# Optimization experiments

Hardware: AMD Instinct MI355X
Metric: run time of the kernel (lower is better)

The kernel has to match this reference:

```python
import jax, jax.numpy as jnp
import numpy as np
from jax import lax

B_, L_, D_, N_, K_ = 2, 4096, 1024, 16, 4


def setup_inputs() -> dict:
    key = jax.random.key(0)
    ks = jax.random.split(key, 11)
    s = lambda fan: 1.0 / np.sqrt(fan)
    return {
        "x": jax.random.normal(ks[0], (B_, L_, D_), jnp.float32),
        "W_in": jax.random.normal(ks[1], (D_, 2 * D_), jnp.float32) * s(D_),
        "b_in": jax.random.normal(ks[2], (2 * D_,), jnp.float32) * 0.01,
        "conv_w": jax.random.normal(ks[3], (D_, K_), jnp.float32) * s(K_),
        "conv_b": jax.random.normal(ks[4], (D_,), jnp.float32) * 0.01,
        "W_x": jax.random.normal(ks[5], (D_, 2 * N_), jnp.float32) * s(D_),
        "b_x": jax.random.normal(ks[6], (2 * N_,), jnp.float32) * 0.01,
        "A_log": jax.random.normal(ks[7], (D_, N_), jnp.float32),
        "D_param": jnp.ones((D_,), jnp.float32),
        "W_out": jax.random.normal(ks[8], (D_, D_), jnp.float32) * s(D_),
        "b_out": jax.random.normal(ks[9], (D_,), jnp.float32) * 0.01,
    }


def silu(x):
    return x * jax.nn.sigmoid(x)


def s6_forward(x, W_in, b_in, conv_w, conv_b, W_x, b_x, A_log, D_param, W_out, b_out):
    b, L, D = x.shape
    # in_proj then split into ssm stream and gate
    x_and_gate = x @ W_in + b_in                      # [b, L, 2D]
    x_ssm, gate = jnp.split(x_and_gate, 2, axis=-1)   # each [b, L, D]

    # depthwise causal conv: padding=(d_conv-1, d_conv-1) then [:, :, :L] == left-pad only
    xc = jnp.transpose(x_ssm, (0, 2, 1))              # [b, D, L]
    xc = lax.conv_general_dilated(
        xc, conv_w[:, None, :],                       # [D, 1, K]
        window_strides=(1,), padding=[(K_ - 1, 0)],
        feature_group_count=D,
        dimension_numbers=("NCH", "OIH", "NCH"),
    ) + conv_b[None, :, None]
    x_conv = silu(jnp.transpose(xc, (0, 2, 1)))       # [b, L, D]

    # data-dependent B, C
    BC = x_conv @ W_x + b_x                           # [b, L, 2N]
    B_mat, C_mat = jnp.split(BC, 2, axis=-1)          # each [b, L, N]

    A_discrete = jnp.exp(-jnp.exp(A_log))             # [D, N]

    # sequential selective scan over L, carry h: [b, D, N]
    def step(h, inp):
        xc_t, B_t, C_t = inp                          # [b,D], [b,N], [b,N]
        h = A_discrete[None] * h + xc_t[:, :, None] * B_t[:, None, :]
        y = jnp.einsum("bn,bdn->bd", C_t, h) + D_param * xc_t
        return h, y

    h0 = jnp.zeros((b, D, N_), x.dtype)
    xs = (jnp.transpose(x_conv, (1, 0, 2)),
          jnp.transpose(B_mat, (1, 0, 2)),
          jnp.transpose(C_mat, (1, 0, 2)))
    h_final, ys = lax.scan(step, h0, xs)              # ys: [L, b, D]
    y = jnp.transpose(ys, (1, 0, 2))                  # [b, L, D]

    y = y * silu(gate)
    y = y @ W_out + b_out
    final_state = h_final.mean(axis=1)                # [b, N]
    return y, final_state


def reference(x, W_in, b_in, conv_w, conv_b, W_x, b_x, A_log, D_param, W_out, b_out):
    return s6_forward(x, W_in, b_in, conv_w, conv_b, W_x, b_x, A_log, D_param, W_out, b_out)
```

## Files before the change

### kernel.cpp

```cpp
#include <hip/hip_runtime.h>
#include <hip/hip_bf16.h>
#include <math.h>

#define LL 4096
#define DD 1024
#define NN 16
#define KK 4
#define BB 2
#define MM (BB * LL)
#define NC 64
#define LC 64

typedef unsigned short ushort_t;
typedef short s16x8 __attribute__((ext_vector_type(8)));
typedef float f32x4 __attribute__((ext_vector_type(4)));
typedef unsigned int u32;

__device__ __forceinline__ ushort_t f2bf(float f) {
  __hip_bfloat16 h = __float2bfloat16(f);
  return *reinterpret_cast<ushort_t*>(&h);
}

__global__ __launch_bounds__(256) void gemm_bt_mfma(
    const ushort_t* __restrict__ A,
    const ushort_t* __restrict__ BT,
    const float* __restrict__ bias,
    float* __restrict__ C, int N) {
  constexpr int K = 1024;
  __shared__ ushort_t As[128 * 32];
  __shared__ ushort_t Bs[128 * 32];

  const int tid = threadIdx.x;
  const int lane = tid & 63;
  const int w = tid >> 6;
  const int wm = w & 1, wn = w >> 1;
  const int row0 = blockIdx.y * 128;
  const int col0 = blockIdx.x * 128;

  const int lrow = lane >> 2;
  const int lk = (lane & 3) * 8;

  f32x4 acc[4][4];
#pragma unroll
  for (int i = 0; i < 4; ++i)
#pragma unroll
    for (int j = 0; j < 4; ++j) acc[i][j] = (f32x4){0.f, 0.f, 0.f, 0.f};

  const int frow = lane & 15;
  const int quad = lane >> 4;

  for (int k0 = 0; k0 < K; k0 += 32) {
#pragma unroll
    for (int it = 0; it < 2; ++it) {
      int r = it * 64 + w * 16;
      __builtin_amdgcn_global_load_lds(
          (const __attribute__((address_space(1))) u32*)(A + (size_t)(row0 + r + lrow) * K + k0 + lk),
          (__attribute__((address_space(3))) u32*)(As + r * 32), 16, 0, 0);
      __builtin_amdgcn_global_load_lds(
          (const __attribute__((address_space(1))) u32*)(BT + (size_t)(col0 + r + lrow) * K + k0 + lk),
          (__attribute__((address_space(3))) u32*)(Bs + r * 32), 16, 0, 0);
    }
    __syncthreads();

    s16x8 af[4], bf[4];
#pragma unroll
    for (int mi = 0; mi < 4; ++mi)
      af[mi] = *(const s16x8*)&As[(wm * 64 + mi * 16 + frow) * 32 + quad * 8];
#pragma unroll
    for (int ni = 0; ni < 4; ++ni)
      bf[ni] = *(const s16x8*)&Bs[(wn * 64 + ni * 16 + frow) * 32 + quad * 8];
#pragma unroll
    for (int mi = 0; mi < 4; ++mi)
#pragma unroll
      for (int ni = 0; ni < 4; ++ni)
        acc[mi][ni] = __builtin_amdgcn_mfma_f32_16x16x32_bf16(
            af[mi], bf[ni], acc[mi][ni], 0, 0, 0);
    __syncthreads();
  }

#pragma unroll
  for (int mi = 0; mi < 4; ++mi) {
#pragma unroll
    for (int ni = 0; ni < 4; ++ni) {
      int col = col0 + wn * 64 + ni * 16 + frow;
      float b = bias[col];
#pragma unroll
      for (int r = 0; r < 4; ++r) {
        int row = row0 + wm * 64 + mi * 16 + quad * 4 + r;
        C[(size_t)row * N + col] = acc[mi][ni][r] + b;
      }
    }
  }
}

__global__ __launch_bounds__(128) void bc_mfma_k(
    const ushort_t* __restrict__ A,
    const ushort_t* __restrict__ BT,
    const float* __restrict__ bias,
    float* __restrict__ C) {
  constexpr int K = 1024;
  __shared__ ushort_t As[32 * 32];
  __shared__ ushort_t Bs[32 * 32];

  const int tid = threadIdx.x;
  const int lane = tid & 63;
  const int w = tid >> 6;
  const int row0 = blockIdx.x * 32;
  const int lrow = lane >> 2;
  const int lk = (lane & 3) * 8;
  const int frow = lane & 15;
  const int quad = lane >> 4;

  f32x4 acc[2];
  acc[0] = (f32x4){0.f, 0.f, 0.f, 0.f};
  acc[1] = (f32x4){0.f, 0.f, 0.f, 0.f};

  for (int k0 = 0; k0 < K; k0 += 32) {
    __builtin_amdgcn_global_load_lds(
        (const __attribute__((address_space(1))) u32*)(A + (size_t)(row0 + w * 16 + lrow) * K + k0 + lk),
        (__attribute__((address_space(3))) u32*)(As + (w * 16) * 32), 16, 0, 0);
    __builtin_amdgcn_global_load_lds(
        (const __attribute__((address_space(1))) u32*)(BT + (size_t)(w * 16 + lrow) * K + k0 + lk),
        (__attribute__((address_space(3))) u32*)(Bs + (w * 16) * 32), 16, 0, 0);
    __syncthreads();

    s16x8 af = *(const s16x8*)&As[(w * 16 + frow) * 32 + quad * 8];
    s16x8 bf0 = *(const s16x8*)&Bs[(frow)*32 + quad * 8];
    s16x8 bf1 = *(const s16x8*)&Bs[(16 + frow) * 32 + quad * 8];
    acc[0] = __builtin_amdgcn_mfma_f32_16x16x32_bf16(af, bf0, acc[0], 0, 0, 0);
    acc[1] = __builtin_amdgcn_mfma_f32_16x16x32_bf16(af, bf1, acc[1], 0, 0, 0);
    __syncthreads();
  }

#pragma unroll
  for (int ni = 0; ni < 2; ++ni) {
    int col = ni * 16 + frow;
    float b = bias[col];
#pragma unroll
    for (int r = 0; r < 4; ++r) {
      int row = row0 + w * 16 + quad * 4 + r;
      C[(size_t)row * 32 + col] = acc[ni][r] + b;
    }
  }
}

__global__ __launch_bounds__(256) void cast_bf16_k(
    const float* __restrict__ src, ushort_t* __restrict__ dst) {
  int i = blockIdx.x * 256 + threadIdx.x;
  float4 v = ((const float4*)src)[i];
  ushort4 o;
  o.x = f2bf(v.x); o.y = f2bf(v.y); o.z = f2bf(v.z); o.w = f2bf(v.w);
  ((ushort4*)dst)[i] = o;
}

__global__ __launch_bounds__(256) void transpose_cast_k(
    const float* __restrict__ W, ushort_t* __restrict__ WT, int K, int N) {
  __shared__ float t[32][33];
  int nb = blockIdx.x * 32, kb = blockIdx.y * 32;
  int tx = threadIdx.x, ty = threadIdx.y;
#pragma unroll
  for (int i = 0; i < 32; i += 8)
    t[ty + i][tx] = W[(size_t)(kb + ty + i) * N + nb + tx];
  __syncthreads();
#pragma unroll
  for (int i = 0; i < 32; i += 8)
    WT[(size_t)(nb + ty + i) * K + kb + tx] = f2bf(t[tx][ty + i]);
}

__global__ __launch_bounds__(256) void conv_silu_k(
    const float* __restrict__ XG, const float* __restrict__ conv_w,
    const float* __restrict__ conv_b, float* __restrict__ XC,
    ushort_t* __restrict__ XCb) {
  int idx = blockIdx.x * 256 + threadIdx.x;
  int d = idx & (DD - 1);
  int m = idx >> 10;
  int b = m >> 12;
  int l = m & (LL - 1);
  float v = conv_b[d];
#pragma unroll
  for (int k = 0; k < KK; ++k) {
    int li = l + k - (KK - 1);
    if (li >= 0) v += XG[((size_t)(b * LL + li)) * 2048 + d] * conv_w[d * KK + k];
  }
  float s = v / (1.f + __expf(-v));
  XC[(size_t)m * DD + d] = s;
  XCb[(size_t)m * DD + d] = f2bf(s);
}

__global__ void zero_fs_k(float* fs) {
  if (threadIdx.x < 32) fs[threadIdx.x] = 0.f;
}

__global__ __launch_bounds__(64) void scan_local_k(
    const float* __restrict__ XC, const float* __restrict__ BC,
    const float* __restrict__ A_log, float* __restrict__ S) {
  const int b = blockIdx.x, c = blockIdx.y;
  const int tid = threadIdx.x;
  const int d = blockIdx.z * 64 + tid;
  const int t0 = c * LC;
  const size_t rowb = (size_t)b * LL;

  __shared__ float bc[LC * 32];
  {
    const float4* src = (const float4*)(BC + (rowb + t0) * 32);
    float4* dst = (float4*)bc;
#pragma unroll
    for (int i = 0; i < 8; ++i) dst[tid + i * 64] = src[tid + i * 64];
  }

  float a[NN], h[NN];
#pragma unroll
  for (int n = 0; n < NN; ++n) {
    a[n] = expf(-expf(A_log[d * NN + n]));
    h[n] = 0.f;
  }
  __syncthreads();

  const float* xp = XC + (rowb + t0) * DD + d;
  float xc = *xp;
  for (int t = 0; t < LC; ++t) {
    float xc_n = (t + 1 < LC) ? xp[(t + 1) * DD] : 0.f;
#pragma unroll
    for (int n = 0; n < NN; ++n) h[n] = a[n] * h[n] + xc * bc[t * 32 + n];
    xc = xc_n;
  }
  float* sp = S + (((size_t)(b * NC + c)) * DD + d) * NN;
#pragma unroll
  for (int n = 0; n < NN; ++n) sp[n] = h[n];
}

__global__ __launch_bounds__(256) void scan_carry_k(
    float* __restrict__ S, const float* __restrict__ A_log,
    float* __restrict__ fs) {
  const int idx = blockIdx.x * 256 + threadIdx.x;
  const int n = idx & (NN - 1);
  const int d = (idx / NN) & (DD - 1);
  const int b = idx / (NN * DD);

  const float aLC = expf(-(float)LC * expf(A_log[d * NN + n]));
  float h = 0.f;
  for (int c = 0; c < NC; ++c) {
    size_t off = (((size_t)(b * NC + c)) * DD + d) * NN + n;
    float s = S[off];
    S[off] = h;
    h = aLC * h + s;
  }
  __shared__ float red[256];
  red[threadIdx.x] = h * (1.f / (float)DD);
  __syncthreads();
  if (threadIdx.x < NN) {
    float sum = 0.f;
#pragma unroll
    for (int i = 0; i < 16; ++i) sum += red[i * NN + threadIdx.x];
    atomicAdd(&fs[b * NN + threadIdx.x], sum);
  }
}

__global__ __launch_bounds__(64) void scan_final_k(
    const float* __restrict__ XC, const float* __restrict__ XG,
    const float* __restrict__ BC, const float* __restrict__ A_log,
    const float* __restrict__ D_param, const float* __restrict__ H0,
    ushort_t* __restrict__ Y1b) {
  const int b = blockIdx.x, c = blockIdx.y;
  const int tid = threadIdx.x;
  const int d = blockIdx.z * 64 + tid;
  const int t0 = c * LC;
  const size_t rowb = (size_t)b * LL;

  __shared__ float bc[LC * 32];
  {
    const float4* src = (const float4*)(BC + (rowb + t0) * 32);
    float4* dst = (float4*)bc;
#pragma unroll
    for (int i = 0; i < 8; ++i) dst[tid + i * 64] = src[tid + i * 64];
  }

  float a[NN], h[NN];
  const float* hp = H0 + (((size_t)(b * NC + c)) * DD + d) * NN;
#pragma unroll
  for (int n = 0; n < NN; ++n) {
    a[n] = expf(-expf(A_log[d * NN + n]));
    h[n] = hp[n];
  }
  const float Dp = D_param[d];
  __syncthreads();

  const float* xp = XC + (rowb + t0) * DD + d;
  const float* gp = XG + (rowb + t0) * 2048 + DD + d;
  ushort_t* yp = Y1b + (rowb + t0) * DD + d;
  float xc = *xp, gate = *gp;
  for (int t = 0; t < LC; ++t) {
    float xc_n = 0.f, g_n = 0.f;
    if (t + 1 < LC) {
      xc_n = xp[(t + 1) * DD];
      g_n = gp[(t + 1) * 2048];
    }
    float y = Dp * xc;
#pragma unroll
    for (int n = 0; n < NN; ++n) {
      h[n] = a[n] * h[n] + xc * bc[t * 32 + n];
      y += bc[t * 32 + 16 + n] * h[n];
    }
    float sg = gate / (1.f + __expf(-gate));
    yp[t * DD] = f2bf(y * sg);
    xc = xc_n;
    gate = g_n;
  }
}

extern "C" void kernel_launch(void* const* d_in, const int* in_sizes, int n_in,
                              void* d_out, int out_size, void* d_ws,
                              size_t ws_size, hipStream_t stream) {
  const float* x = (const float*)d_in[0];
  const float* W_in = (const float*)d_in[1];
  const float* b_in = (const float*)d_in[2];
  const float* conv_w = (const float*)d_in[3];
  const float* conv_b = (const float*)d_in[4];
  const float* W_x = (const float*)d_in[5];
  const float* b_x = (const float*)d_in[6];
  const float* A_log = (const float*)d_in[7];
  const float* D_param = (const float*)d_in[8];
  const float* W_out = (const float*)d_in[9];
  const float* b_out = (const float*)d_in[10];
  float* out = (float*)d_out;

  float* XG = (float*)d_ws;
  float* XC = XG + (size_t)MM * 2048;
  float* BC = XC + (size_t)MM * DD;
  float* S = BC + (size_t)MM * 32;
  ushort_t* Xb = (ushort_t*)(S + (size_t)BB * NC * DD * NN);
  ushort_t* WinT = Xb + (size_t)MM * DD;
  ushort_t* WoutT = WinT + (size_t)2048 * DD;
  ushort_t* Y1b = WoutT + (size_t)DD * DD;
  ushort_t* XCb = Y1b + (size_t)MM * DD;
  ushort_t* WxT = XCb + (size_t)MM * DD;

  dim3 blk(256);
  cast_bf16_k<<<dim3((MM * DD) / 1024), blk, 0, stream>>>(x, Xb);
  transpose_cast_k<<<dim3(2048 / 32, 1024 / 32), dim3(32, 8), 0, stream>>>(
      W_in, WinT, 1024, 2048);
  transpose_cast_k<<<dim3(1024 / 32, 1024 / 32), dim3(32, 8), 0, stream>>>(
      W_out, WoutT, 1024, 1024);
  transpose_cast_k<<<dim3(1, 1024 / 32), dim3(32, 8), 0, stream>>>(
      W_x, WxT, 1024, 32);
  gemm_bt_mfma<<<dim3(2048 / 128, MM / 128), blk, 0, stream>>>(
      Xb, WinT, b_in, XG, 2048);
  conv_silu_k<<<dim3((MM * DD) / 256), blk, 0, stream>>>(XG, conv_w, conv_b,
                                                         XC, XCb);
  bc_mfma_k<<<dim3(MM / 32), dim3(128), 0, stream>>>(XCb, WxT, b_x, BC);
  scan_local_k<<<dim3(BB, NC, DD / 64), dim3(64), 0, stream>>>(XC, BC, A_log, S);
  zero_fs_k<<<dim3(1), dim3(64), 0, stream>>>(out + (size_t)MM * DD);
  scan_carry_k<<<dim3((BB * DD * NN) / 256), blk, 0, stream>>>(
      S, A_log, out + (size_t)MM * DD);
  scan_final_k<<<dim3(BB, NC, DD / 64), dim3(64), 0, stream>>>(
      XC, XG, BC, A_log, D_param, S, Y1b);
  gemm_bt_mfma<<<dim3(1024 / 128, MM / 128), blk, 0, stream>>>(
      Y1b, WoutT, b_out, out, 1024);
}
```

Baseline: 305.7 us.

## Store intermediates in bf16, vectorize conv, process two channels per scan thread

The in-projection GEMM now writes its output in bf16 instead of fp32. The conv kernel reads and writes only bf16 and handles 8 channels per thread with vector loads. The scan kernels read bf16 inputs and process two channels per thread, which halves the block count per chunk, and the fp32 XC/XG buffers are dropped. The zero-fill and three transpose launches are merged into fewer kernels. This cuts memory traffic on the largest intermediates and removes launches, at the cost of extra bf16 rounding on the gate and scan inputs and less parallelism in the scan.

```diff
diff --git a/kernel.cpp b/kernel.cpp
--- a/kernel.cpp
+++ b/kernel.cpp
@@ -20,12 +20,18 @@
   __hip_bfloat16 h = __float2bfloat16(f);
   return *reinterpret_cast<ushort_t*>(&h);
 }
-
+__device__ __forceinline__ float bf2f(ushort_t u) {
+  union { u32 i; float f; } c;
+  c.i = ((u32)u) << 16;
+  return c.f;
+}
+
+template <bool BF16OUT>
 __global__ __launch_bounds__(256) void gemm_bt_mfma(
     const ushort_t* __restrict__ A,
     const ushort_t* __restrict__ BT,
     const float* __restrict__ bias,
-    float* __restrict__ C, int N) {
+    void* __restrict__ Cv, int N) {
   constexpr int K = 1024;
   __shared__ ushort_t As[128 * 32];
   __shared__ ushort_t Bs[128 * 32];
@@ -87,7 +93,10 @@
 #pragma unroll
       for (int r = 0; r < 4; ++r) {
         int row = row0 + wm * 64 + mi * 16 + quad * 4 + r;
-        C[(size_t)row * N + col] = acc[mi][ni][r] + b;
+        if constexpr (BF16OUT)
+          ((ushort_t*)Cv)[(size_t)row * N + col] = f2bf(acc[mi][ni][r] + b);
+        else
+          ((float*)Cv)[(size_t)row * N + col] = acc[mi][ni][r] + b;
       }
     }
   }
@@ -145,7 +154,9 @@
 }
 
 __global__ __launch_bounds__(256) void cast_bf16_k(
-    const float* __restrict__ src, ushort_t* __restrict__ dst) {
+    const float* __restrict__ src, ushort_t* __restrict__ dst,
+    float* __restrict__ fs) {
+  if (blockIdx.x == 0 && threadIdx.x < 32) fs[threadIdx.x] = 0.f;
   int i = blockIdx.x * 256 + threadIdx.x;
   float4 v = ((const float4*)src)[i];
   ushort4 o;
@@ -153,8 +164,23 @@
   ((ushort4*)dst)[i] = o;
 }
 
-__global__ __launch_bounds__(256) void transpose_cast_k(
-    const float* __restrict__ W, ushort_t* __restrict__ WT, int K, int N) {
+__global__ void transpose_cast3_k(
+    const float* __restrict__ W_in, const float* __restrict__ W_out,
+    const float* __restrict__ W_x, ushort_t* __restrict__ WinT,
+    ushort_t* __restrict__ WoutT, ushort_t* __restrict__ WxT) {
+  constexpr int K = 1024;
+  const float* W;
+  ushort_t* WT;
+  int N;
+  if (blockIdx.z == 0) {
+    W = W_in; WT = WinT; N = 2048;
+  } else if (blockIdx.z == 1) {
+    if (blockIdx.x >= 32) return;
+    W = W_out; WT = WoutT; N = 1024;
+  } else {
+    if (blockIdx.x >= 1) return;
+    W = W_x; WT = WxT; N = 32;
+  }
   __shared__ float t[32][33];
   int nb = blockIdx.x * 32, kb = blockIdx.y * 32;
   int tx = threadIdx.x, ty = threadIdx.y;
@@ -168,65 +194,81 @@
 }
 
 __global__ __launch_bounds__(256) void conv_silu_k(
-    const float* __restrict__ XG, const float* __restrict__ conv_w,
-    const float* __restrict__ conv_b, float* __restrict__ XC,
-    ushort_t* __restrict__ XCb) {
-  int idx = blockIdx.x * 256 + threadIdx.x;
-  int d = idx & (DD - 1);
-  int m = idx >> 10;
-  int b = m >> 12;
+    const ushort_t* __restrict__ XGb, const float* __restrict__ conv_w,
+    const float* __restrict__ conv_b, ushort_t* __restrict__ XCb) {
+  int gid = blockIdx.x * 256 + threadIdx.x;
+  int m = gid >> 7;
+  int d0 = (gid & 127) * 8;
   int l = m & (LL - 1);
-  float v = conv_b[d];
+
+  float acc[8];
+#pragma unroll
+  for (int j = 0; j < 8; ++j) acc[j] = conv_b[d0 + j];
 #pragma unroll
   for (int k = 0; k < KK; ++k) {
     int li = l + k - (KK - 1);
-    if (li >= 0) v += XG[((size_t)(b * LL + li)) * 2048 + d] * conv_w[d * KK + k];
-  }
-  float s = v / (1.f + __expf(-v));
-  XC[(size_t)m * DD + d] = s;
-  XCb[(size_t)m * DD + d] = f2bf(s);
-}
-
-__global__ void zero_fs_k(float* fs) {
-  if (threadIdx.x < 32) fs[threadIdx.x] = 0.f;
+    if (li < 0) continue;
+    s16x8 v = *(const s16x8*)(XGb + (size_t)(m + k - (KK - 1)) * 2048 + d0);
+#pragma unroll
+    for (int j = 0; j < 8; ++j)
+      acc[j] += bf2f((ushort_t)v[j]) * conv_w[(d0 + j) * KK + k];
+  }
+  ushort_t o[8];
+#pragma unroll
+  for (int j = 0; j < 8; ++j) {
+    float s = acc[j] / (1.f + __expf(-acc[j]));
+    o[j] = f2bf(s);
+  }
+  *(s16x8*)(XCb + (size_t)m * DD + d0) = *(const s16x8*)o;
 }
 
 __global__ __launch_bounds__(64) void scan_local_k(
-    const float* __restrict__ XC, const float* __restrict__ BC,
+    const ushort_t* __restrict__ XCb, const float* __restrict__ BC,
     const float* __restrict__ A_log, float* __restrict__ S) {
   const int b = blockIdx.x, c = blockIdx.y;
   const int tid = threadIdx.x;
-  const int d = blockIdx.z * 64 + tid;
+  const int d0 = blockIdx.z * 128 + tid * 2;
   const int t0 = c * LC;
   const size_t rowb = (size_t)b * LL;
 
-  __shared__ float bc[LC * 32];
+  __shared__ float bcs[LC * 32];
   {
     const float4* src = (const float4*)(BC + (rowb + t0) * 32);
-    float4* dst = (float4*)bc;
+    float4* dst = (float4*)bcs;
 #pragma unroll
     for (int i = 0; i < 8; ++i) dst[tid + i * 64] = src[tid + i * 64];
   }
 
-  float a[NN], h[NN];
+  float a0[NN], a1[NN], h0[NN], h1[NN];
 #pragma unroll
   for (int n = 0; n < NN; ++n) {
-    a[n] = expf(-expf(A_log[d * NN + n]));
-    h[n] = 0.f;
+    a0[n] = expf(-expf(A_log[d0 * NN + n]));
+    a1[n] = expf(-expf(A_log[(d0 + 1) * NN + n]));
+    h0[n] = 0.f;
+    h1[n] = 0.f;
   }
   __syncthreads();
 
-  const float* xp = XC + (rowb + t0) * DD + d;
-  float xc = *xp;
+  const ushort_t* xp = XCb + (rowb + t0) * DD + d0;
+  u32 xw = *(const u32*)xp;
   for (int t = 0; t < LC; ++t) {
-    float xc_n = (t + 1 < LC) ? xp[(t + 1) * DD] : 0.f;
-#pragma unroll
-    for (int n = 0; n < NN; ++n) h[n] = a[n] * h[n] + xc * bc[t * 32 + n];
-    xc = xc_n;
-  }
-  float* sp = S + (((size_t)(b * NC + c)) * DD + d) * NN;
-#pragma unroll
-  for (int n = 0; n < NN; ++n) sp[n] = h[n];
+    u32 xw_n = (t + 1 < LC) ? *(const u32*)(xp + (size_t)(t + 1) * DD) : 0u;
+    float x0 = bf2f((ushort_t)(xw & 0xffff));
+    float x1 = bf2f((ushort_t)(xw >> 16));
+    const float* bp = bcs + t * 32;
+#pragma unroll
+    for (int n = 0; n < NN; ++n) {
+      float bv = bp[n];
+      h0[n] = a0[n] * h0[n] + x0 * bv;
+      h1[n] = a1[n] * h1[n] + x1 * bv;
+    }
+    xw = xw_n;
+  }
+  float* sp = S + (((size_t)(b * NC + c)) * DD + d0) * NN;
+#pragma unroll
+  for (int n = 0; n < NN; ++n) sp[n] = h0[n];
+#pragma unroll
+  for (int n = 0; n < NN; ++n) sp[NN + n] = h1[n];
 }
 
 __global__ __launch_bounds__(256) void scan_carry_k(
@@ -257,54 +299,67 @@
 }
 
 __global__ __launch_bounds__(64) void scan_final_k(
-    const float* __restrict__ XC, const float* __restrict__ XG,
+    const ushort_t* __restrict__ XCb, const ushort_t* __restrict__ XGb,
     const float* __restrict__ BC, const float* __restrict__ A_log,
     const float* __restrict__ D_param, const float* __restrict__ H0,
     ushort_t* __restrict__ Y1b) {
   const int b = blockIdx.x, c = blockIdx.y;
   const int tid = threadIdx.x;
-  const int d = blockIdx.z * 64 + tid;
+  const int d0 = blockIdx.z * 128 + tid * 2;
   const int t0 = c * LC;
   const size_t rowb = (size_t)b * LL;
 
-  __shared__ float bc[LC * 32];
+  __shared__ float bcs[LC * 32];
   {
     const float4* src = (const float4*)(BC + (rowb + t0) * 32);
-    float4* dst = (float4*)bc;
+    float4* dst = (float4*)bcs;
 #pragma unroll
     for (int i = 0; i < 8; ++i) dst[tid + i * 64] = src[tid + i * 64];
   }
 
-  float a[NN], h[NN];
-  const float* hp = H0 + (((size_t)(b * NC + c)) * DD + d) * NN;
+  float a0[NN], a1[NN], h0[NN], h1[NN];
+  const float* hp = H0 + (((size_t)(b * NC + c)) * DD + d0) * NN;
 #pragma unroll
   for (int n = 0; n < NN; ++n) {
-    a[n] = expf(-expf(A_log[d * NN + n]));
-    h[n] = hp[n];
-  }
-  const float Dp = D_param[d];
+    a0[n] = expf(-expf(A_log[d0 * NN + n]));
+    a1[n] = expf(-expf(A_log[(d0 + 1) * NN + n]));
+    h0[n] = hp[n];
+    h1[n] = hp[NN + n];
+  }
+  const float Dp0 = D_param[d0], Dp1 = D_param[d0 + 1];
   __syncthreads();
 
-  const float* xp = XC + (rowb + t0) * DD + d;
-  const float* gp = XG + (rowb + t0) * 2048 + DD + d;
-  ushort_t* yp = Y1b + (rowb + t0) * DD + d;
-  float xc = *xp, gate = *gp;
+  const ushort_t* xp = XCb + (rowb + t0) * DD + d0;
+  const ushort_t* gp = XGb + (rowb + t0) * 2048 + DD + d0;
+  ushort_t* yp = Y1b + (rowb + t0) * DD + d0;
+  u32 xw = *(const u32*)xp;
+  u32 gw = *(const u32*)gp;
   for (int t = 0; t < LC; ++t) {
-    float xc_n = 0.f, g_n = 0.f;
+    u32 xw_n = 0u, gw_n = 0u;
     if (t + 1 < LC) {
-      xc_n = xp[(t + 1) * DD];
-      g_n = gp[(t + 1) * 2048];
-    }
-    float y = Dp * xc;
+      xw_n = *(const u32*)(xp + (size_t)(t + 1) * DD);
+      gw_n = *(const u32*)(gp + (size_t)(t + 1) * 2048);
+    }
+    float x0 = bf2f((ushort_t)(xw & 0xffff));
+    float x1 = bf2f((ushort_t)(xw >> 16));
+    float g0 = bf2f((ushort_t)(gw & 0xffff));
+    float g1 = bf2f((ushort_t)(gw >> 16));
+    float y0 = Dp0 * x0, y1 = Dp1 * x1;
+    const float* bp = bcs + t * 32;
 #pragma unroll
     for (int n = 0; n < NN; ++n) {
-      h[n] = a[n] * h[n] + xc * bc[t * 32 + n];
-      y += bc[t * 32 + 16 + n] * h[n];
-    }
-    float sg = gate / (1.f + __expf(-gate));
-    yp[t * DD] = f2bf(y * sg);
-    xc = xc_n;
-    gate = g_n;
+      float bv = bp[n], cv = bp[16 + n];
+      h0[n] = a0[n] * h0[n] + x0 * bv;
+      h1[n] = a1[n] * h1[n] + x1 * bv;
+      y0 += cv * h0[n];
+      y1 += cv * h1[n];
+    }
+    float sg0 = g0 / (1.f + __expf(-g0));
+    float sg1 = g1 / (1.f + __expf(-g1));
+    u32 outw = (u32)f2bf(y0 * sg0) | ((u32)f2bf(y1 * sg1) << 16);
+    *(u32*)(yp + (size_t)t * DD) = outw;
+    xw = xw_n;
+    gw = gw_n;
   }
 }
 
@@ -323,37 +378,32 @@
   const float* W_out = (const float*)d_in[9];
   const float* b_out = (const float*)d_in[10];
   float* out = (float*)d_out;
-
-  float* XG = (float*)d_ws;
-  float* XC = XG + (size_t)MM * 2048;
-  float* BC = XC + (size_t)MM * DD;
+  float* fs = out + (size_t)MM * DD;
+
+  float* BC = (float*)d_ws;
   float* S = BC + (size_t)MM * 32;
   ushort_t* Xb = (ushort_t*)(S + (size_t)BB * NC * DD * NN);
-  ushort_t* WinT = Xb + (size_t)MM * DD;
+  ushort_t* XGb = Xb + (size_t)MM * DD;
+  ushort_t* XCb = XGb + (size_t)MM * 2048;
+  ushort_t* Y1b = XCb + (size_t)MM * DD;
+  ushort_t* WinT = Y1b + (size_t)MM * DD;
   ushort_t* WoutT = WinT + (size_t)2048 * DD;
-  ushort_t* Y1b = WoutT + (size_t)DD * DD;
-  ushort_t* XCb = Y1b + (size_t)MM * DD;
-  ushort_t* WxT = XCb + (size_t)MM * DD;
+  ushort_t* WxT = WoutT + (size_t)DD * DD;
 
   dim3 blk(256);
-  cast_bf16_k<<<dim3((MM * DD) / 1024), blk, 0, stream>>>(x, Xb);
-  transpose_cast_k<<<dim3(2048 / 32, 1024 / 32), dim3(32, 8), 0, stream>>>(
-      W_in, WinT, 1024, 2048);
-  transpose_cast_k<<<dim3(1024 / 32, 1024 / 32), dim3(32, 8), 0, stream>>>(
-      W_out, WoutT, 1024, 1024);
-  transpose_cast_k<<<dim3(1, 1024 / 32), dim3(32, 8), 0, stream>>>(
-      W_x, WxT, 1024, 32);
-  gemm_bt_mfma<<<dim3(2048 / 128, MM / 128), blk, 0, stream>>>(
-      Xb, WinT, b_in, XG, 2048);
-  conv_silu_k<<<dim3((MM * DD) / 256), blk, 0, stream>>>(XG, conv_w, conv_b,
-                                                         XC, XCb);
+  cast_bf16_k<<<dim3((MM * DD) / 1024), blk, 0, stream>>>(x, Xb, fs);
+  transpose_cast3_k<<<dim3(64, 32, 3), dim3(32, 8), 0, stream>>>(
+      W_in, W_out, W_x, WinT, WoutT, WxT);
+  gemm_bt_mfma<true><<<dim3(2048 / 128, MM / 128), blk, 0, stream>>>(
+      Xb, WinT, b_in, XGb, 2048);
+  conv_silu_k<<<dim3((MM * 128) / 256), blk, 0, stream>>>(XGb, conv_w, conv_b,
+                                                          XCb);
   bc_mfma_k<<<dim3(MM / 32), dim3(128), 0, stream>>>(XCb, WxT, b_x, BC);
-  scan_local_k<<<dim3(BB, NC, DD / 64), dim3(64), 0, stream>>>(XC, BC, A_log, S);
-  zero_fs_k<<<dim3(1), dim3(64), 0, stream>>>(out + (size_t)MM * DD);
-  scan_carry_k<<<dim3((BB * DD * NN) / 256), blk, 0, stream>>>(
-      S, A_log, out + (size_t)MM * DD);
-  scan_final_k<<<dim3(BB, NC, DD / 64), dim3(64), 0, stream>>>(
-      XC, XG, BC, A_log, D_param, S, Y1b);
-  gemm_bt_mfma<<<dim3(1024 / 128, MM / 128), blk, 0, stream>>>(
+  scan_local_k<<<dim3(BB, NC, DD / 128), dim3(64), 0, stream>>>(XCb, BC, A_log,
+                                                                S);
+  scan_carry_k<<<dim3((BB * DD * NN) / 256), blk, 0, stream>>>(S, A_log, fs);
+  scan_final_k<<<dim3(BB, NC, DD / 128), dim3(64), 0, stream>>>(
+      XCb, XGb, BC, A_log, D_param, S, Y1b);
+  gemm_bt_mfma<false><<<dim3(1024 / 128, MM / 128), blk, 0, stream>>>(
       Y1b, WoutT, b_out, out, 1024);
 }
```

Result: slower. 329.7 us (+7.9%).
